# Kernel tuning notes

Hardware: AMD Instinct MI355X
Metric: run time of the kernel (lower is better)

## Reference

```python
import jax, jax.numpy as jnp
import numpy as np

D, HEADS, LVLS, PTS, DFF = 256, 8, 4, 4, 1024
LQ, B = 900, 16
SHAPES = [(100, 100), (50, 50), (25, 25), (13, 13)]
S = sum(h * w for h, w in SHAPES)  # 13294
EPS = 1e-5


def layer_norm(x, g, b):
    m = jnp.mean(x, -1, keepdims=True)
    v = jnp.mean((x - m) ** 2, -1, keepdims=True)
    return (x - m) * jax.lax.rsqrt(v + EPS) * g + b


def bilinear_gather(value_l, loc, H_, W_):
    # value_l: (b,h,H_,W_,dh); loc: (b,h,Lq,P,2) normalized to [0,1]
    b, h, _, _, dh = value_l.shape
    Lq, P = loc.shape[2], loc.shape[3]
    # grid_sample align_corners=False, padding_mode='zeros' semantics
    x = loc[..., 0] * W_ - 0.5
    y = loc[..., 1] * H_ - 0.5
    x0 = jnp.floor(x); y0 = jnp.floor(y)
    wx = x - x0; wy = y - y0
    x0i = x0.astype(jnp.int32); y0i = y0.astype(jnp.int32)
    vflat = value_l.reshape(b, h, H_ * W_, dh)

    def corner(xi, yi, w):
        valid = (xi >= 0) & (xi < W_) & (yi >= 0) & (yi < H_)
        idx = jnp.clip(yi, 0, H_ - 1) * W_ + jnp.clip(xi, 0, W_ - 1)
        g = jnp.take_along_axis(vflat, idx.reshape(b, h, Lq * P)[..., None], axis=2)
        return g.reshape(b, h, Lq, P, dh) * (w * valid)[..., None]

    return (corner(x0i, y0i, (1 - wx) * (1 - wy)) + corner(x0i + 1, y0i, wx * (1 - wy))
            + corner(x0i, y0i + 1, (1 - wx) * wy) + corner(x0i + 1, y0i + 1, wx * wy))


def setup_inputs() -> dict:
    key = jax.random.key(0)
    ks = jax.random.split(key, 32)
    w = lambda k, *s: (jax.random.normal(k, s, jnp.float32) * 0.02)
    shapes = jnp.array(SHAPES, jnp.int32)
    starts = jnp.array(np.cumsum([0] + [h_ * w_ for h_, w_ in SHAPES[:-1]]), jnp.int32)
    return {
        'tgt': jax.random.normal(ks[0], (LQ, B, D), jnp.float32),
        'tgt_query_pos': jax.random.normal(ks[1], (LQ, B, D), jnp.float32),
        'tgt_reference_points': jax.random.uniform(ks[2], (LQ, B, LVLS, 4), jnp.float32, 0.05, 0.95),
        'memory': jax.random.normal(ks[3], (S, B, D), jnp.float32),
        'memory_spatial_shapes': shapes,
        'memory_level_start_index': starts,
        # self-attn (nn.MultiheadAttention)
        'in_proj_w': w(ks[4], 3 * D, D), 'in_proj_b': jnp.zeros((3 * D,), jnp.float32),
        'sa_out_w': w(ks[5], D, D), 'sa_out_b': jnp.zeros((D,), jnp.float32),
        # MSDeformAttn
        'off_w': w(ks[6], HEADS * LVLS * PTS * 2, D), 'off_b': w(ks[7], HEADS * LVLS * PTS * 2),
        'aw_w': w(ks[8], HEADS * LVLS * PTS, D), 'aw_b': jnp.zeros((HEADS * LVLS * PTS,), jnp.float32),
        'val_w': w(ks[9], D, D), 'val_b': jnp.zeros((D,), jnp.float32),
        'ca_out_w': w(ks[10], D, D), 'ca_out_b': jnp.zeros((D,), jnp.float32),
        # FFN
        'lin1_w': w(ks[11], DFF, D), 'lin1_b': jnp.zeros((DFF,), jnp.float32),
        'lin2_w': w(ks[12], D, DFF), 'lin2_b': jnp.zeros((D,), jnp.float32),
        # norms (norm2 after sa, norm1 after ca, norm3 after ffn)
        'norm1_g': jnp.ones((D,), jnp.float32), 'norm1_b': jnp.zeros((D,), jnp.float32),
        'norm2_g': jnp.ones((D,), jnp.float32), 'norm2_b': jnp.zeros((D,), jnp.float32),
        'norm3_g': jnp.ones((D,), jnp.float32), 'norm3_b': jnp.zeros((D,), jnp.float32),
    }


def reference(tgt, tgt_query_pos, tgt_reference_points, memory,
              memory_spatial_shapes, memory_level_start_index,
              in_proj_w, in_proj_b, sa_out_w, sa_out_b,
              off_w, off_b, aw_w, aw_b, val_w, val_b, ca_out_w, ca_out_b,
              lin1_w, lin1_b, lin2_w, lin2_b,
              norm1_g, norm1_b, norm2_g, norm2_b, norm3_g, norm3_b):
    Lq, b, d = tgt.shape
    h = HEADS
    dh = d // h
    shapes = np.asarray(memory_spatial_shapes)  # static level shapes
    starts = np.asarray(memory_level_start_index)

    # ---- self-attention (module_seq[0] = 'sa') ----
    qk = tgt + tgt_query_pos  # pos on q,k only
    Wq, Wk, Wv = jnp.split(in_proj_w, 3, axis=0)
    bq, bk, bv = jnp.split(in_proj_b, 3)
    to_heads = lambda x: x.transpose(1, 0, 2).reshape(b, Lq, h, dh).transpose(0, 2, 1, 3)
    qh = to_heads(qk @ Wq.T + bq)
    kh = to_heads(qk @ Wk.T + bk)
    vh = to_heads(tgt @ Wv.T + bv)
    attn = jax.nn.softmax(jnp.einsum('bhqd,bhkd->bhqk', qh, kh) / jnp.sqrt(jnp.float32(dh)), axis=-1)
    sa = jnp.einsum('bhqk,bhkd->bhqd', attn, vh).transpose(0, 2, 1, 3).reshape(b, Lq, d).transpose(1, 0, 2)
    sa = sa @ sa_out_w.T + sa_out_b
    tgt = layer_norm(tgt + sa, norm2_g, norm2_b)

    # ---- deformable cross-attention (MSDeformAttn) ----
    query = (tgt + tgt_query_pos).transpose(1, 0, 2)            # (b,Lq,d)
    ref = tgt_reference_points.transpose(1, 0, 2, 3)            # (b,Lq,L,4)
    value = (memory.transpose(1, 0, 2) @ val_w.T + val_b).reshape(b, -1, h, dh)  # (b,S,h,dh)
    off = (query @ off_w.T + off_b).reshape(b, Lq, h, LVLS, PTS, 2)
    aw = jax.nn.softmax((query @ aw_w.T + aw_b).reshape(b, Lq, h, LVLS * PTS), axis=-1)
    aw = aw.reshape(b, Lq, h, LVLS, PTS).transpose(0, 2, 1, 3, 4)  # (b,h,Lq,L,P)
    # 4-dim refs: loc = xy + off/P * wh * 0.5
    loc = ref[:, :, None, :, None, :2] + off / PTS * ref[:, :, None, :, None, 2:] * 0.5
    loc = loc.transpose(0, 2, 1, 3, 4, 5)                        # (b,h,Lq,L,P,2)

    out = jnp.zeros((b, h, Lq, dh), jnp.float32)
    for l in range(LVLS):
        H_, W_ = int(shapes[l, 0]), int(shapes[l, 1])
        s0 = int(starts[l])
        value_l = value[:, s0:s0 + H_ * W_].reshape(b, H_, W_, h, dh).transpose(0, 3, 1, 2, 4)
        samp = bilinear_gather(value_l, loc[:, :, :, l], H_, W_)   # (b,h,Lq,P,dh)
        out = out + jnp.einsum('bhqpd,bhqp->bhqd', samp, aw[:, :, :, l])
    ca = out.transpose(0, 2, 1, 3).reshape(b, Lq, d) @ ca_out_w.T + ca_out_b
    ca = ca.transpose(1, 0, 2)
    tgt = layer_norm(tgt + ca, norm1_g, norm1_b)

    # ---- FFN (intended math: linear2(relu(linear1(tgt)))) ----
    t2 = jnp.maximum(tgt @ lin1_w.T + lin1_b, 0.0) @ lin2_w.T + lin2_b
    tgt = layer_norm(tgt + t2, norm3_g, norm3_b)
    return tgt
```

## Files before the change

### kernel.cpp

```cpp
#include <hip/hip_runtime.h>
#include <hip/hip_bf16.h>
#include <math.h>

#define D_ 256
#define HEADS_ 8
#define DH_ 32
#define LVLS_ 4
#define PTS_ 4
#define DFF_ 1024
#define LQ_ 900
#define B_ 16
#define S_ 13294
#define MQ (LQ_*B_)
#define MV (S_*B_)

typedef __attribute__((ext_vector_type(4))) float f32x4;
typedef __attribute__((ext_vector_type(8))) short bf16x8;

static __device__ inline ushort f2bf(float f) {
  __hip_bfloat16 h = __float2bfloat16(f);
  union { __hip_bfloat16 h; ushort u; } c; c.h = h;
  return c.u;
}
static __device__ inline float bf2f(ushort u) {
  union { float f; uint u; } c; c.u = (uint)u << 16; return c.f;
}

#define GP 40

__global__ __launch_bounds__(512) void gemm_bf16_512(
    const float* __restrict__ A, const float* __restrict__ Wm,
    const float* __restrict__ bias, float* __restrict__ Y,
    int M, int N, int K, int relu, int outbf)
{
  __shared__ ushort As[128 * GP];
  __shared__ ushort Ws[128 * GP];
  const int tid  = threadIdx.x;
  const int lane = tid & 63;
  const int wid  = tid >> 6;
  const int wr   = wid >> 1;
  const int wc   = wid & 1;
  const int fr = lane & 15;
  const int fk = (lane >> 4) << 3;
  const int m0 = blockIdx.y * 128, n0 = blockIdx.x * 128;

  f32x4 acc[2][4];
  const f32x4 zero = {0.f, 0.f, 0.f, 0.f};
#pragma unroll
  for (int i = 0; i < 2; ++i)
#pragma unroll
    for (int j = 0; j < 4; ++j) acc[i][j] = zero;

  const int srow = tid >> 2;
  const int skh  = (tid & 3) << 3;
  int agr = m0 + srow; if (agr > M - 1) agr = M - 1;
  const float* apb = A  + (size_t)agr * K + skh;
  const float* wpb = Wm + (size_t)(n0 + srow) * K + skh;

  float4 pa[2], pw[2];
  pa[0] = *(const float4*)(apb);     pa[1] = *(const float4*)(apb + 4);
  pw[0] = *(const float4*)(wpb);     pw[1] = *(const float4*)(wpb + 4);

  for (int k0 = 0; k0 < K; k0 += 32) {
    if (k0) __syncthreads();
    ushort tmp[8] __attribute__((aligned(16)));
    tmp[0]=f2bf(pa[0].x); tmp[1]=f2bf(pa[0].y); tmp[2]=f2bf(pa[0].z); tmp[3]=f2bf(pa[0].w);
    tmp[4]=f2bf(pa[1].x); tmp[5]=f2bf(pa[1].y); tmp[6]=f2bf(pa[1].z); tmp[7]=f2bf(pa[1].w);
    *(bf16x8*)&As[srow*GP + skh] = *(const bf16x8*)tmp;
    tmp[0]=f2bf(pw[0].x); tmp[1]=f2bf(pw[0].y); tmp[2]=f2bf(pw[0].z); tmp[3]=f2bf(pw[0].w);
    tmp[4]=f2bf(pw[1].x); tmp[5]=f2bf(pw[1].y); tmp[6]=f2bf(pw[1].z); tmp[7]=f2bf(pw[1].w);
    *(bf16x8*)&Ws[srow*GP + skh] = *(const bf16x8*)tmp;
    if (k0 + 32 < K) {
      const float* ap = apb + k0 + 32;
      const float* wp = wpb + k0 + 32;
      pa[0] = *(const float4*)(ap);  pa[1] = *(const float4*)(ap + 4);
      pw[0] = *(const float4*)(wp);  pw[1] = *(const float4*)(wp + 4);
    }
    __syncthreads();

    bf16x8 ar[2], br[4];
#pragma unroll
    for (int i = 0; i < 2; ++i)
      ar[i] = *(const bf16x8*)&As[(wr*32 + i*16 + fr)*GP + fk];
#pragma unroll
    for (int j = 0; j < 4; ++j)
      br[j] = *(const bf16x8*)&Ws[(wc*64 + j*16 + fr)*GP + fk];
#pragma unroll
    for (int i = 0; i < 2; ++i)
#pragma unroll
      for (int j = 0; j < 4; ++j)
        acc[i][j] = __builtin_amdgcn_mfma_f32_16x16x32_bf16(ar[i], br[j], acc[i][j], 0, 0, 0);
  }

  const int gcolbase = n0 + wc * 64 + fr;
  float bias4[4];
#pragma unroll
  for (int j = 0; j < 4; ++j) bias4[j] = bias[gcolbase + j * 16];
#pragma unroll
  for (int i = 0; i < 2; ++i) {
    const int rb = m0 + wr * 32 + i * 16 + (lane >> 4) * 4;
#pragma unroll
    for (int r = 0; r < 4; ++r) {
      const int grow = rb + r;
      if (grow < M) {
#pragma unroll
        for (int j = 0; j < 4; ++j) {
          float v = acc[i][j][r] + bias4[j];
          if (relu) v = fmaxf(v, 0.f);
          if (outbf) ((ushort*)Y)[(size_t)grow * N + gcolbase + j * 16] = f2bf(v);
          else       Y[(size_t)grow * N + gcolbase + j * 16] = v;
        }
      }
    }
  }
}

__global__ __launch_bounds__(256) void gemm_bf16_64(
    const float* __restrict__ A, const float* __restrict__ X2,
    const float* __restrict__ Wm, const float* __restrict__ bias,
    float* __restrict__ Y, int M, int N, int K, int relu, int outbf)
{
  __shared__ ushort As[64 * GP];
  __shared__ ushort Ws[64 * GP];
  const int tid  = threadIdx.x;
  const int lane = tid & 63;
  const int wid  = tid >> 6;
  const int wr = wid >> 1, wc = wid & 1;
  const int fr = lane & 15;
  const int fk = (lane >> 4) << 3;
  const int m0 = blockIdx.y * 64, n0 = blockIdx.x * 64;

  f32x4 acc[2][2];
  const f32x4 zero = {0.f, 0.f, 0.f, 0.f};
#pragma unroll
  for (int i = 0; i < 2; ++i)
#pragma unroll
    for (int j = 0; j < 2; ++j) acc[i][j] = zero;

  const int srow = tid >> 1;
  const int skh  = (tid & 1) << 4;
  const bool isA = srow < 64;
  const float* src;
  const float* src2 = nullptr;
  ushort* dst;
  if (isA) {
    int gr = m0 + srow; if (gr > M - 1) gr = M - 1;
    src = A + (size_t)gr * K + skh;
    if (X2) src2 = X2 + (size_t)gr * K + skh;
    dst = &As[srow * GP + skh];
  } else {
    src = Wm + (size_t)(n0 + srow - 64) * K + skh;
    dst = &Ws[(srow - 64) * GP + skh];
  }

  float4 pd[4];
#pragma unroll
  for (int i2 = 0; i2 < 4; ++i2) pd[i2] = *(const float4*)(src + i2 * 4);
  if (src2) {
#pragma unroll
    for (int i2 = 0; i2 < 4; ++i2) {
      const float4 u = *(const float4*)(src2 + i2 * 4);
      pd[i2].x += u.x; pd[i2].y += u.y; pd[i2].z += u.z; pd[i2].w += u.w;
    }
  }

  for (int k0 = 0; k0 < K; k0 += 32) {
    if (k0) __syncthreads();
    ushort tmp[16] __attribute__((aligned(16)));
#pragma unroll
    for (int i2 = 0; i2 < 4; ++i2) {
      tmp[i2*4+0] = f2bf(pd[i2].x); tmp[i2*4+1] = f2bf(pd[i2].y);
      tmp[i2*4+2] = f2bf(pd[i2].z); tmp[i2*4+3] = f2bf(pd[i2].w);
    }
    *(bf16x8*)(dst)     = *(const bf16x8*)&tmp[0];
    *(bf16x8*)(dst + 8) = *(const bf16x8*)&tmp[8];
    if (k0 + 32 < K) {
      const float* s = src + k0 + 32;
#pragma unroll
      for (int i2 = 0; i2 < 4; ++i2) pd[i2] = *(const float4*)(s + i2 * 4);
      if (src2) {
        const float* s2 = src2 + k0 + 32;
#pragma unroll
        for (int i2 = 0; i2 < 4; ++i2) {
          const float4 u = *(const float4*)(s2 + i2 * 4);
          pd[i2].x += u.x; pd[i2].y += u.y; pd[i2].z += u.z; pd[i2].w += u.w;
        }
      }
    }
    __syncthreads();

    bf16x8 af[2], bf[2];
#pragma unroll
    for (int i = 0; i < 2; ++i)
      af[i] = *(const bf16x8*)&As[(wr*32 + i*16 + fr)*GP + fk];
#pragma unroll
    for (int j = 0; j < 2; ++j)
      bf[j] = *(const bf16x8*)&Ws[(wc*32 + j*16 + fr)*GP + fk];
#pragma unroll
    for (int i = 0; i < 2; ++i)
#pragma unroll
      for (int j = 0; j < 2; ++j)
        acc[i][j] = __builtin_amdgcn_mfma_f32_16x16x32_bf16(af[i], bf[j], acc[i][j], 0, 0, 0);
  }

  const int gcolbase = n0 + wc * 32 + fr;
  float bias2[2];
#pragma unroll
  for (int j = 0; j < 2; ++j) bias2[j] = bias[gcolbase + j * 16];
#pragma unroll
  for (int i = 0; i < 2; ++i) {
    const int rb = m0 + wr * 32 + i * 16 + (lane >> 4) * 4;
#pragma unroll
    for (int r = 0; r < 4; ++r) {
      const int grow = rb + r;
      if (grow < M) {
#pragma unroll
        for (int j = 0; j < 2; ++j) {
          float v = acc[i][j][r] + bias2[j];
          if (relu) v = fmaxf(v, 0.f);
          if (outbf) ((ushort*)Y)[(size_t)grow * N + gcolbase + j * 16] = f2bf(v);
          else       Y[(size_t)grow * N + gcolbase + j * 16] = v;
        }
      }
    }
  }
}

#define QB 64
#define KB 64
#define KP 40
#define VP 72
__global__ __launch_bounds__(256) void attn_mfma_kernel(
    const float* __restrict__ QK, const float* __restrict__ V,
    float* __restrict__ O)
{
  __shared__ ushort Ks[KB * KP];
  __shared__ ushort Vt[DH_ * VP];
  __shared__ ushort Pl[4][16 * KP];
  const int tid  = threadIdx.x;
  const int lane = tid & 63;
  const int w    = tid >> 6;
  const int bh = blockIdx.y;
  const int h  = bh & (HEADS_ - 1);
  const int b  = bh >> 3;
  const int q0 = blockIdx.x * QB;
  const int lq = lane & 15;
  const int lg = lane >> 4;
  const float scale = 0.17677669529663687f;
  const f32x4 zero4 = {0.f, 0.f, 0.f, 0.f};

  bf16x8 qf;
  {
    int qg = q0 + w * 16 + lq; if (qg > LQ_ - 1) qg = LQ_ - 1;
    const float* qp = QK + ((size_t)qg * B_ + b) * 512 + h * DH_ + lg * 8;
    const float4 a = *(const float4*)qp;
    const float4 c = *(const float4*)(qp + 4);
    ushort t[8] __attribute__((aligned(16)));
    t[0]=f2bf(a.x*scale); t[1]=f2bf(a.y*scale); t[2]=f2bf(a.z*scale); t[3]=f2bf(a.w*scale);
    t[4]=f2bf(c.x*scale); t[5]=f2bf(c.y*scale); t[6]=f2bf(c.z*scale); t[7]=f2bf(c.w*scale);
    qf = *(const bf16x8*)t;
  }

  float mrow = -1e30f, srow = 0.f;
  f32x4 oacc[2]; oacc[0] = zero4; oacc[1] = zero4;

  const int nkt = (LQ_ + KB - 1) / KB;
  for (int t = 0; t < nkt; ++t) {
    const int k0 = t * KB;
    const int klen = (LQ_ - k0) < KB ? (LQ_ - k0) : KB;
    if (t) __syncthreads();
    {
      const int kk  = tid >> 2;
      const int dh0 = (tid & 3) * 8;
      ushort kb[8] __attribute__((aligned(16)));
      ushort vb[8];
      if (kk < klen) {
        const size_t row = (size_t)(k0 + kk) * B_ + b;
        const float* kp = QK + row * 512 + 256 + h * DH_ + dh0;
        const float* vp = V  + row * 256 + h * DH_ + dh0;
        const float4 k1 = *(const float4*)kp;
        const float4 k2 = *(const float4*)(kp + 4);
        const float4 v1 = *(const float4*)vp;
        const float4 v2 = *(const float4*)(vp + 4);
        kb[0]=f2bf(k1.x); kb[1]=f2bf(k1.y); kb[2]=f2bf(k1.z); kb[3]=f2bf(k1.w);
        kb[4]=f2bf(k2.x); kb[5]=f2bf(k2.y); kb[6]=f2bf(k2.z); kb[7]=f2bf(k2.w);
        vb[0]=f2bf(v1.x); vb[1]=f2bf(v1.y); vb[2]=f2bf(v1.z); vb[3]=f2bf(v1.w);
        vb[4]=f2bf(v2.x); vb[5]=f2bf(v2.y); vb[6]=f2bf(v2.z); vb[7]=f2bf(v2.w);
      } else {
#pragma unroll
        for (int j = 0; j < 8; ++j) { kb[j] = 0; vb[j] = 0; }
      }
      *(bf16x8*)&Ks[kk * KP + dh0] = *(const bf16x8*)kb;
#pragma unroll
      for (int j = 0; j < 8; ++j) Vt[(dh0 + j) * VP + kk] = vb[j];
    }
    __syncthreads();

    f32x4 sc[4];
#pragma unroll
    for (int j = 0; j < 4; ++j) {
      const bf16x8 kf = *(const bf16x8*)&Ks[(j * 16 + lq) * KP + lg * 8];
      sc[j] = __builtin_amdgcn_mfma_f32_16x16x32_bf16(kf, qf, zero4, 0, 0, 0);
    }
    if (klen < KB) {
#pragma unroll
      for (int j = 0; j < 4; ++j)
#pragma unroll
        for (int r = 0; r < 4; ++r)
          if (j * 16 + lg * 4 + r >= klen) sc[j][r] = -1e30f;
    }
    float tmax = -1e30f;
#pragma unroll
    for (int j = 0; j < 4; ++j)
#pragma unroll
      for (int r = 0; r < 4; ++r) tmax = fmaxf(tmax, sc[j][r]);
    tmax = fmaxf(tmax, __shfl_xor(tmax, 16, 64));
    tmax = fmaxf(tmax, __shfl_xor(tmax, 32, 64));
    const float mnew = fmaxf(mrow, tmax);
    const float cfac = __expf(mrow - mnew);
    mrow = mnew;
    float tsum = 0.f;
#pragma unroll
    for (int j = 0; j < 4; ++j)
#pragma unroll
      for (int r = 0; r < 4; ++r) {
        const float p = __expf(sc[j][r] - mnew);
        sc[j][r] = p; tsum += p;
      }
    tsum += __shfl_xor(tsum, 16, 64);
    tsum += __shfl_xor(tsum, 32, 64);
    srow = srow * cfac + tsum;
#pragma unroll
    for (int j = 0; j < 4; ++j) {
      const uint lo = (uint)f2bf(sc[j][0]) | ((uint)f2bf(sc[j][1]) << 16);
      const uint hi = (uint)f2bf(sc[j][2]) | ((uint)f2bf(sc[j][3]) << 16);
      *(uint*)&Pl[w][lq * KP + j * 16 + lg * 4]     = lo;
      *(uint*)&Pl[w][lq * KP + j * 16 + lg * 4 + 2] = hi;
    }
    float crow[4];
#pragma unroll
    for (int r = 0; r < 4; ++r) crow[r] = __shfl(cfac, lg * 4 + r, 64);
#pragma unroll
    for (int nt = 0; nt < 2; ++nt)
#pragma unroll
      for (int r = 0; r < 4; ++r) oacc[nt][r] *= crow[r];
#pragma unroll
    for (int ks = 0; ks < 2; ++ks) {
      const bf16x8 pf = *(const bf16x8*)&Pl[w][lq * KP + ks * 32 + lg * 8];
#pragma unroll
      for (int nt = 0; nt < 2; ++nt) {
        const bf16x8 vf = *(const bf16x8*)&Vt[(nt * 16 + lq) * VP + ks * 32 + lg * 8];
        oacc[nt] = __builtin_amdgcn_mfma_f32_16x16x32_bf16(pf, vf, oacc[nt], 0, 0, 0);
      }
    }
  }
  float sinv[4];
#pragma unroll
  for (int r = 0; r < 4; ++r) {
    const float sr = __shfl(srow, lg * 4 + r, 64);
    sinv[r] = 1.f / sr;
  }
#pragma unroll
  for (int r = 0; r < 4; ++r) {
    const int qg = q0 + w * 16 + lg * 4 + r;
    if (qg < LQ_) {
      float* op = O + ((size_t)qg * B_ + b) * 256 + h * DH_;
      op[lq]      = oacc[0][r] * sinv[r];
      op[16 + lq] = oacc[1][r] * sinv[r];
    }
  }
}

__global__ __launch_bounds__(256) void ln_kernel(
    const float* __restrict__ X, const float* __restrict__ R,
    const float* __restrict__ g, const float* __restrict__ be,
    float* __restrict__ Y)
{
  const int row  = blockIdx.x * 4 + (threadIdx.x >> 6);
  const int lane = threadIdx.x & 63;
  const size_t base = (size_t)row * D_ + lane * 4;
  float4 v = *(const float4*)(X + base);
  const float4 rv = *(const float4*)(R + base);
  v.x += rv.x; v.y += rv.y; v.z += rv.z; v.w += rv.w;

  float sum = (v.x + v.y) + (v.z + v.w);
#pragma unroll
  for (int o = 32; o > 0; o >>= 1) sum += __shfl_xor(sum, o, 64);
  const float mean = sum * (1.f / D_);
  const float4 d = make_float4(v.x - mean, v.y - mean, v.z - mean, v.w - mean);
  float sq = (d.x * d.x + d.y * d.y) + (d.z * d.z + d.w * d.w);
#pragma unroll
  for (int o = 32; o > 0; o >>= 1) sq += __shfl_xor(sq, o, 64);
  const float rs = rsqrtf(sq * (1.f / D_) + 1e-5f);

  const float4 gv = *(const float4*)(g + lane * 4);
  const float4 bv = *(const float4*)(be + lane * 4);
  float4 o4;
  o4.x = d.x * rs * gv.x + bv.x;
  o4.y = d.y * rs * gv.y + bv.y;
  o4.z = d.z * rs * gv.z + bv.z;
  o4.w = d.w * rs * gv.w + bv.w;
  *(float4*)(Y + base) = o4;
}

__global__ __launch_bounds__(256) void msdeform_kernel(
    const float* __restrict__ refp, const float* __restrict__ offb,
    const float* __restrict__ awb, const ushort* __restrict__ value,
    float* __restrict__ out)
{
  const int t  = blockIdx.x * 256 + threadIdx.x;
  const int dq = t & 3;
  const int h  = (t >> 2) & 7;
  const int u  = t >> 5;
  const int b  = u / LQ_;
  const int q  = u - b * LQ_;
  const int r  = q * B_ + b;

  float aw[LVLS_ * PTS_];
  const float* ap = awb + (size_t)r * 128 + h * 16;
  float m = -1e30f;
#pragma unroll
  for (int i = 0; i < 16; ++i) { aw[i] = ap[i]; m = fmaxf(m, aw[i]); }
  float s = 0.f;
#pragma unroll
  for (int i = 0; i < 16; ++i) { aw[i] = __expf(aw[i] - m); s += aw[i]; }
  const float inv = 1.f / s;
#pragma unroll
  for (int i = 0; i < 16; ++i) aw[i] *= inv;

  float o[8] = {};
  const int HH[4] = {100, 50, 25, 13};
  const int WW[4] = {100, 50, 25, 13};
  const int ST[4] = {0, 10000, 12500, 13125};
  const float* orow = offb + (size_t)r * 256 + h * (LVLS_ * PTS_ * 2);
  const int dh0 = h * DH_ + dq * 8;

  for (int l = 0; l < LVLS_; ++l) {
    const float4 rf = *(const float4*)(refp + (((size_t)q * B_ + b) * LVLS_ + l) * 4);
    const int W_ = WW[l], H_ = HH[l], s0 = ST[l];
    for (int p = 0; p < PTS_; ++p) {
      const float ox = orow[(l * PTS_ + p) * 2 + 0];
      const float oy = orow[(l * PTS_ + p) * 2 + 1];
      const float lx = rf.x + ox * 0.125f * rf.z;
      const float ly = rf.y + oy * 0.125f * rf.w;
      const float x = lx * W_ - 0.5f;
      const float y = ly * H_ - 0.5f;
      const float x0f = floorf(x), y0f = floorf(y);
      const float wx = x - x0f, wy = y - y0f;
      const int x0 = (int)x0f, y0 = (int)y0f;
      const float a = aw[l * PTS_ + p];
      const float cw[4] = {(1.f - wx) * (1.f - wy) * a, wx * (1.f - wy) * a,
                           (1.f - wx) * wy * a,         wx * wy * a};
      const int cx[4] = {x0, x0 + 1, x0, x0 + 1};
      const int cy[4] = {y0, y0, y0 + 1, y0 + 1};
#pragma unroll
      for (int c = 0; c < 4; ++c) {
        const int xi = cx[c], yi = cy[c];
        if (xi >= 0 && xi < W_ && yi >= 0 && yi < H_) {
          const ushort* vp = value + ((size_t)(s0 + yi * W_ + xi) * B_ + b) * 256 + dh0;
          const float w = cw[c];
          const bf16x8 vv = *(const bf16x8*)vp;
#pragma unroll
          for (int j = 0; j < 8; ++j)
            o[j] = fmaf(w, bf2f(((const ushort*)&vv)[j]), o[j]);
        }
      }
    }
  }
  float* op = out + (size_t)r * 256 + dh0;
  float4 x1; x1.x = o[0]; x1.y = o[1]; x1.z = o[2]; x1.w = o[3];
  float4 x2; x2.x = o[4]; x2.y = o[5]; x2.z = o[6]; x2.w = o[7];
  *(float4*)op = x1;
  *(float4*)(op + 4) = x2;
}

extern "C" void kernel_launch(void* const* d_in, const int* in_sizes, int n_in,
                              void* d_out, int out_size, void* d_ws, size_t ws_size,
                              hipStream_t stream) {
  const float* tgt       = (const float*)d_in[0];
  const float* pos       = (const float*)d_in[1];
  const float* refp      = (const float*)d_in[2];
  const float* memory    = (const float*)d_in[3];
  const float* in_proj_w = (const float*)d_in[6];
  const float* in_proj_b = (const float*)d_in[7];
  const float* sa_out_w  = (const float*)d_in[8];
  const float* sa_out_b  = (const float*)d_in[9];
  const float* off_w     = (const float*)d_in[10];
  const float* off_b     = (const float*)d_in[11];
  const float* aw_w      = (const float*)d_in[12];
  const float* aw_b      = (const float*)d_in[13];
  const float* val_w     = (const float*)d_in[14];
  const float* val_b     = (const float*)d_in[15];
  const float* ca_out_w  = (const float*)d_in[16];
  const float* ca_out_b  = (const float*)d_in[17];
  const float* lin1_w    = (const float*)d_in[18];
  const float* lin1_b    = (const float*)d_in[19];
  const float* lin2_w    = (const float*)d_in[20];
  const float* lin2_b    = (const float*)d_in[21];
  const float* n1g = (const float*)d_in[22];
  const float* n1b = (const float*)d_in[23];
  const float* n2g = (const float*)d_in[24];
  const float* n2b = (const float*)d_in[25];
  const float* n3g = (const float*)d_in[26];
  const float* n3b = (const float*)d_in[27];

  float* ws = (float*)d_ws;
  float* QK    = ws;
  float* Vb    = QK   + (size_t)MQ * 512;
  float* Cb    = Vb   + (size_t)MQ * 256;
  float* Db    = Cb   + (size_t)MQ * 256;
  float* tgt1  = Db   + (size_t)MQ * 256;
  float* tgt2  = tgt1 + (size_t)MQ * 256;
  float* big   = tgt2 + (size_t)MQ * 256;
  ushort* value = (ushort*)big;
  float* mid   = big;

  const dim3 blk(256);
  const int gy_q = (MQ + 63) / 64;
  const int gy_v128 = (MV + 127) / 128;
  const int qtiles = (LQ_ + QB - 1) / QB;

  gemm_bf16_64<<<dim3(8, gy_q), blk, 0, stream>>>(tgt, pos, in_proj_w, in_proj_b, QK, MQ, 512, D_, 0, 0);
  gemm_bf16_64<<<dim3(4, gy_q), blk, 0, stream>>>(tgt, nullptr, in_proj_w + 512 * D_, in_proj_b + 512, Vb, MQ, 256, D_, 0, 0);
  attn_mfma_kernel<<<dim3(qtiles, B_ * HEADS_), blk, 0, stream>>>(QK, Vb, Cb);
  gemm_bf16_64<<<dim3(4, gy_q), blk, 0, stream>>>(Cb, nullptr, sa_out_w, sa_out_b, Db, MQ, 256, D_, 0, 0);
  ln_kernel<<<MQ / 4, blk, 0, stream>>>(tgt, Db, n2g, n2b, tgt1);
  gemm_bf16_512<<<dim3(2, gy_v128), dim3(512), 0, stream>>>(memory, val_w, val_b, (float*)value, MV, 256, D_, 0, 1);
  gemm_bf16_64<<<dim3(4, gy_q), blk, 0, stream>>>(tgt1, pos, off_w, off_b, QK, MQ, 256, D_, 0, 0);
  gemm_bf16_64<<<dim3(2, gy_q), blk, 0, stream>>>(tgt1, pos, aw_w, aw_b, Vb, MQ, 128, D_, 0, 0);
  msdeform_kernel<<<(MQ * HEADS_ * 4 + 255) / 256, blk, 0, stream>>>(refp, QK, Vb, value, Cb);
  gemm_bf16_64<<<dim3(4, gy_q), blk, 0, stream>>>(Cb, nullptr, ca_out_w, ca_out_b, Db, MQ, 256, D_, 0, 0);
  ln_kernel<<<MQ / 4, blk, 0, stream>>>(tgt1, Db, n1g, n1b, tgt2);
  gemm_bf16_64<<<dim3(16, gy_q), blk, 0, stream>>>(tgt2, nullptr, lin1_w, lin1_b, mid, MQ, DFF_, D_, 1, 0);
  gemm_bf16_64<<<dim3(4, gy_q), blk, 0, stream>>>(mid, nullptr, lin2_w, lin2_b, Db, MQ, 256, DFF_, 0, 0);
  ln_kernel<<<MQ / 4, blk, 0, stream>>>(tgt2, Db, n3g, n3b, (float*)d_out);
}
```

Measured before the change: 528.3 us.

## Process two query subtiles per wave in self-attention and pack V transpose stores

Each wave of the self-attention kernel now handles 32 queries (two 16-row subtiles) instead of 16, so the block query tile grows from 64 to 128. Each K/V tile staged in shared memory is reused across twice as many queries, which halves global K/V loads and bf16 conversions per query. The V transpose into shared memory is rewritten so each thread loads two key rows and writes packed 32-bit pairs instead of scalar 16-bit stores. The change doubles per-wave accumulator and register state and halves the grid (8 query blocks instead of 15), which may reduce occupancy and leave some compute units idle.

```diff
diff --git a/kernel.cpp b/kernel.cpp
--- a/kernel.cpp
+++ b/kernel.cpp
@@ -226,7 +226,7 @@
   }
 }
 
-#define QB 64
+#define QB 128
 #define KB 64
 #define KP 40
 #define VP 72
@@ -236,7 +236,7 @@
 {
   __shared__ ushort Ks[KB * KP];
   __shared__ ushort Vt[DH_ * VP];
-  __shared__ ushort Pl[4][16 * KP];
+  __shared__ ushort Pl[4][32 * KP];
   const int tid  = threadIdx.x;
   const int lane = tid & 63;
   const int w    = tid >> 6;
@@ -249,20 +249,22 @@
   const float scale = 0.17677669529663687f;
   const f32x4 zero4 = {0.f, 0.f, 0.f, 0.f};
 
-  bf16x8 qf;
-  {
-    int qg = q0 + w * 16 + lq; if (qg > LQ_ - 1) qg = LQ_ - 1;
+  bf16x8 qf[2];
+#pragma unroll
+  for (int s = 0; s < 2; ++s) {
+    int qg = q0 + w * 32 + s * 16 + lq; if (qg > LQ_ - 1) qg = LQ_ - 1;
     const float* qp = QK + ((size_t)qg * B_ + b) * 512 + h * DH_ + lg * 8;
     const float4 a = *(const float4*)qp;
     const float4 c = *(const float4*)(qp + 4);
     ushort t[8] __attribute__((aligned(16)));
     t[0]=f2bf(a.x*scale); t[1]=f2bf(a.y*scale); t[2]=f2bf(a.z*scale); t[3]=f2bf(a.w*scale);
     t[4]=f2bf(c.x*scale); t[5]=f2bf(c.y*scale); t[6]=f2bf(c.z*scale); t[7]=f2bf(c.w*scale);
-    qf = *(const bf16x8*)t;
-  }
-
-  float mrow = -1e30f, srow = 0.f;
-  f32x4 oacc[2]; oacc[0] = zero4; oacc[1] = zero4;
+    qf[s] = *(const bf16x8*)t;
+  }
+
+  float mrow[2] = {-1e30f, -1e30f}, srow[2] = {0.f, 0.f};
+  f32x4 oacc[2][2];
+  oacc[0][0] = zero4; oacc[0][1] = zero4; oacc[1][0] = zero4; oacc[1][1] = zero4;
 
   const int nkt = (LQ_ + KB - 1) / KB;
   for (int t = 0; t < nkt; ++t) {
@@ -273,100 +275,120 @@
       const int kk  = tid >> 2;
       const int dh0 = (tid & 3) * 8;
       ushort kb[8] __attribute__((aligned(16)));
-      ushort vb[8];
       if (kk < klen) {
-        const size_t row = (size_t)(k0 + kk) * B_ + b;
-        const float* kp = QK + row * 512 + 256 + h * DH_ + dh0;
-        const float* vp = V  + row * 256 + h * DH_ + dh0;
+        const float* kp = QK + ((size_t)(k0 + kk) * B_ + b) * 512 + 256 + h * DH_ + dh0;
         const float4 k1 = *(const float4*)kp;
         const float4 k2 = *(const float4*)(kp + 4);
-        const float4 v1 = *(const float4*)vp;
-        const float4 v2 = *(const float4*)(vp + 4);
         kb[0]=f2bf(k1.x); kb[1]=f2bf(k1.y); kb[2]=f2bf(k1.z); kb[3]=f2bf(k1.w);
         kb[4]=f2bf(k2.x); kb[5]=f2bf(k2.y); kb[6]=f2bf(k2.z); kb[7]=f2bf(k2.w);
-        vb[0]=f2bf(v1.x); vb[1]=f2bf(v1.y); vb[2]=f2bf(v1.z); vb[3]=f2bf(v1.w);
-        vb[4]=f2bf(v2.x); vb[5]=f2bf(v2.y); vb[6]=f2bf(v2.z); vb[7]=f2bf(v2.w);
       } else {
 #pragma unroll
-        for (int j = 0; j < 8; ++j) { kb[j] = 0; vb[j] = 0; }
+        for (int j = 0; j < 8; ++j) kb[j] = 0;
       }
       *(bf16x8*)&Ks[kk * KP + dh0] = *(const bf16x8*)kb;
-#pragma unroll
-      for (int j = 0; j < 8; ++j) Vt[(dh0 + j) * VP + kk] = vb[j];
+    }
+    {
+      const int kk2  = (tid >> 3) << 1;
+      const int dh0v = (tid & 7) * 4;
+      float v0[4] = {0.f, 0.f, 0.f, 0.f};
+      float v1[4] = {0.f, 0.f, 0.f, 0.f};
+      if (kk2 < klen) {
+        const float4 x = *(const float4*)(V + ((size_t)(k0 + kk2) * B_ + b) * 256 + h * DH_ + dh0v);
+        v0[0] = x.x; v0[1] = x.y; v0[2] = x.z; v0[3] = x.w;
+      }
+      if (kk2 + 1 < klen) {
+        const float4 x = *(const float4*)(V + ((size_t)(k0 + kk2 + 1) * B_ + b) * 256 + h * DH_ + dh0v);
+        v1[0] = x.x; v1[1] = x.y; v1[2] = x.z; v1[3] = x.w;
+      }
+#pragma unroll
+      for (int j = 0; j < 4; ++j) {
+        const uint pk = (uint)f2bf(v0[j]) | ((uint)f2bf(v1[j]) << 16);
+        *(uint*)&Vt[(dh0v + j) * VP + kk2] = pk;
+      }
     }
     __syncthreads();
 
-    f32x4 sc[4];
-#pragma unroll
-    for (int j = 0; j < 4; ++j) {
-      const bf16x8 kf = *(const bf16x8*)&Ks[(j * 16 + lq) * KP + lg * 8];
-      sc[j] = __builtin_amdgcn_mfma_f32_16x16x32_bf16(kf, qf, zero4, 0, 0, 0);
-    }
-    if (klen < KB) {
+    float cfac[2];
+#pragma unroll
+    for (int s = 0; s < 2; ++s) {
+      f32x4 sc[4];
+#pragma unroll
+      for (int j = 0; j < 4; ++j) {
+        const bf16x8 kf = *(const bf16x8*)&Ks[(j * 16 + lq) * KP + lg * 8];
+        sc[j] = __builtin_amdgcn_mfma_f32_16x16x32_bf16(kf, qf[s], zero4, 0, 0, 0);
+      }
+      if (klen < KB) {
+#pragma unroll
+        for (int j = 0; j < 4; ++j)
+#pragma unroll
+          for (int r = 0; r < 4; ++r)
+            if (j * 16 + lg * 4 + r >= klen) sc[j][r] = -1e30f;
+      }
+      float tmax = -1e30f;
 #pragma unroll
       for (int j = 0; j < 4; ++j)
 #pragma unroll
-        for (int r = 0; r < 4; ++r)
-          if (j * 16 + lg * 4 + r >= klen) sc[j][r] = -1e30f;
-    }
-    float tmax = -1e30f;
-#pragma unroll
-    for (int j = 0; j < 4; ++j)
-#pragma unroll
-      for (int r = 0; r < 4; ++r) tmax = fmaxf(tmax, sc[j][r]);
-    tmax = fmaxf(tmax, __shfl_xor(tmax, 16, 64));
-    tmax = fmaxf(tmax, __shfl_xor(tmax, 32, 64));
-    const float mnew = fmaxf(mrow, tmax);
-    const float cfac = __expf(mrow - mnew);
-    mrow = mnew;
-    float tsum = 0.f;
-#pragma unroll
-    for (int j = 0; j < 4; ++j)
-#pragma unroll
-      for (int r = 0; r < 4; ++r) {
-        const float p = __expf(sc[j][r] - mnew);
-        sc[j][r] = p; tsum += p;
-      }
-    tsum += __shfl_xor(tsum, 16, 64);
-    tsum += __shfl_xor(tsum, 32, 64);
-    srow = srow * cfac + tsum;
-#pragma unroll
-    for (int j = 0; j < 4; ++j) {
-      const uint lo = (uint)f2bf(sc[j][0]) | ((uint)f2bf(sc[j][1]) << 16);
-      const uint hi = (uint)f2bf(sc[j][2]) | ((uint)f2bf(sc[j][3]) << 16);
-      *(uint*)&Pl[w][lq * KP + j * 16 + lg * 4]     = lo;
-      *(uint*)&Pl[w][lq * KP + j * 16 + lg * 4 + 2] = hi;
-    }
-    float crow[4];
-#pragma unroll
-    for (int r = 0; r < 4; ++r) crow[r] = __shfl(cfac, lg * 4 + r, 64);
-#pragma unroll
-    for (int nt = 0; nt < 2; ++nt)
-#pragma unroll
-      for (int r = 0; r < 4; ++r) oacc[nt][r] *= crow[r];
-#pragma unroll
-    for (int ks = 0; ks < 2; ++ks) {
-      const bf16x8 pf = *(const bf16x8*)&Pl[w][lq * KP + ks * 32 + lg * 8];
-#pragma unroll
-      for (int nt = 0; nt < 2; ++nt) {
-        const bf16x8 vf = *(const bf16x8*)&Vt[(nt * 16 + lq) * VP + ks * 32 + lg * 8];
-        oacc[nt] = __builtin_amdgcn_mfma_f32_16x16x32_bf16(pf, vf, oacc[nt], 0, 0, 0);
-      }
-    }
-  }
-  float sinv[4];
-#pragma unroll
-  for (int r = 0; r < 4; ++r) {
-    const float sr = __shfl(srow, lg * 4 + r, 64);
-    sinv[r] = 1.f / sr;
-  }
-#pragma unroll
-  for (int r = 0; r < 4; ++r) {
-    const int qg = q0 + w * 16 + lg * 4 + r;
-    if (qg < LQ_) {
-      float* op = O + ((size_t)qg * B_ + b) * 256 + h * DH_;
-      op[lq]      = oacc[0][r] * sinv[r];
-      op[16 + lq] = oacc[1][r] * sinv[r];
+        for (int r = 0; r < 4; ++r) tmax = fmaxf(tmax, sc[j][r]);
+      tmax = fmaxf(tmax, __shfl_xor(tmax, 16, 64));
+      tmax = fmaxf(tmax, __shfl_xor(tmax, 32, 64));
+      const float mnew = fmaxf(mrow[s], tmax);
+      cfac[s] = __expf(mrow[s] - mnew);
+      mrow[s] = mnew;
+      float tsum = 0.f;
+#pragma unroll
+      for (int j = 0; j < 4; ++j)
+#pragma unroll
+        for (int r = 0; r < 4; ++r) {
+          const float p = __expf(sc[j][r] - mnew);
+          sc[j][r] = p; tsum += p;
+        }
+      tsum += __shfl_xor(tsum, 16, 64);
+      tsum += __shfl_xor(tsum, 32, 64);
+      srow[s] = srow[s] * cfac[s] + tsum;
+#pragma unroll
+      for (int j = 0; j < 4; ++j) {
+        const uint lo = (uint)f2bf(sc[j][0]) | ((uint)f2bf(sc[j][1]) << 16);
+        const uint hi = (uint)f2bf(sc[j][2]) | ((uint)f2bf(sc[j][3]) << 16);
+        *(uint*)&Pl[w][(s * 16 + lq) * KP + j * 16 + lg * 4]     = lo;
+        *(uint*)&Pl[w][(s * 16 + lq) * KP + j * 16 + lg * 4 + 2] = hi;
+      }
+    }
+#pragma unroll
+    for (int s = 0; s < 2; ++s) {
+      float crow[4];
+#pragma unroll
+      for (int r = 0; r < 4; ++r) crow[r] = __shfl(cfac[s], lg * 4 + r, 64);
+#pragma unroll
+      for (int nt = 0; nt < 2; ++nt)
+#pragma unroll
+        for (int r = 0; r < 4; ++r) oacc[s][nt][r] *= crow[r];
+#pragma unroll
+      for (int ks = 0; ks < 2; ++ks) {
+        const bf16x8 pf = *(const bf16x8*)&Pl[w][(s * 16 + lq) * KP + ks * 32 + lg * 8];
+#pragma unroll
+        for (int nt = 0; nt < 2; ++nt) {
+          const bf16x8 vf = *(const bf16x8*)&Vt[(nt * 16 + lq) * VP + ks * 32 + lg * 8];
+          oacc[s][nt] = __builtin_amdgcn_mfma_f32_16x16x32_bf16(pf, vf, oacc[s][nt], 0, 0, 0);
+        }
+      }
+    }
+  }
+#pragma unroll
+  for (int s = 0; s < 2; ++s) {
+    float sinv[4];
+#pragma unroll
+    for (int r = 0; r < 4; ++r) {
+      const float sr = __shfl(srow[s], lg * 4 + r, 64);
+      sinv[r] = 1.f / sr;
+    }
+#pragma unroll
+    for (int r = 0; r < 4; ++r) {
+      const int qg = q0 + w * 32 + s * 16 + lg * 4 + r;
+      if (qg < LQ_) {
+        float* op = O + ((size_t)qg * B_ + b) * 256 + h * DH_;
+        op[lq]      = oacc[s][0][r] * sinv[r];
+        op[16 + lq] = oacc[s][1][r] * sinv[r];
+      }
     }
   }
 }
```

Measured after the change: 522.8 us. Within noise of the previous version (-1.0%).
